# Kernel tuning notes

Measured on AMD Instinct MI355X. Metric: run time of the kernel, lower is better.

Reference implementation:

```python
import jax, jax.numpy as jnp
import numpy as np

N = 20000      # total nodes (100 graphs x 200 nodes)
B = 100        # batch_size
PER = 200      # nodes per graph (uniform) -> max_num_nodes
E = 320000     # edges (before self-loops)
F_IN = 32      # num_features
HEADS = 10
OUT = 128      # output_dim
NEG_SLOPE = 0.2  # PyG GATConv default


def setup_inputs() -> dict:
    key = jax.random.key(0)
    ks = jax.random.split(key, 14)
    feats = jax.random.normal(ks[0], (N, F_IN), jnp.float32)
    src = jax.random.randint(ks[1], (E,), 0, N)
    dst = jax.random.randint(ks[2], (E,), 0, N)
    edge_index = jnp.stack([src, dst]).astype(jnp.int32)
    graph_id = jnp.repeat(jnp.arange(B, dtype=jnp.int32), PER)
    batch_num_nodes = jnp.full((B,), PER, jnp.int32)
    s1 = 1.0 / np.sqrt(F_IN)
    s2 = 1.0 / np.sqrt(F_IN * HEADS)
    s3 = 1.0 / np.sqrt(OUT)
    return {
        "feats": feats,
        "edge_index": edge_index,
        "graph_id": graph_id,
        "batch_num_nodes": batch_num_nodes,
        # GATConv 1: in F_IN -> HEADS x F_IN, concat
        "W1": jax.random.normal(ks[3], (F_IN, HEADS * F_IN), jnp.float32) * s1,
        "a1_src": jax.random.normal(ks[4], (HEADS, F_IN), jnp.float32) * s1,
        "a1_dst": jax.random.normal(ks[5], (HEADS, F_IN), jnp.float32) * s1,
        "b1": jnp.zeros((HEADS * F_IN,), jnp.float32),
        "W2": jax.random.normal(ks[6], (HEADS * F_IN, OUT), jnp.float32) * s2,
        "a2_src": jax.random.normal(ks[7], (1, OUT), jnp.float32) * s3,
        "a2_dst": jax.random.normal(ks[8], (1, OUT), jnp.float32) * s3,
        "b2": jnp.zeros((OUT,), jnp.float32),
        # shared fc_g1
        "fc_w": jax.random.normal(ks[9], (OUT, OUT), jnp.float32) * s3,
        "fc_b": jnp.zeros((OUT,), jnp.float32),
    }


def gat_conv(x, src, dst, W, a_src, a_dst, bias, heads, out_dim):
    # x: [N, Fin]; src/dst already include self-loops (PyG default add_self_loops=True)
    n = x.shape[0]
    xw = (x @ W).reshape(n, heads, out_dim)                 # [N,H,F]
    s_src = jnp.einsum('nhf,hf->nh', xw, a_src)             # [N,H]
    s_dst = jnp.einsum('nhf,hf->nh', xw, a_dst)
    e = jax.nn.leaky_relu(s_src[src] + s_dst[dst], NEG_SLOPE)  # [E,H]
    # segment softmax over incoming edges of each destination node
    m = jax.ops.segment_max(e, dst, num_segments=n)         # [N,H]
    ex = jnp.exp(e - m[dst])
    denom = jax.ops.segment_sum(ex, dst, num_segments=n)    # [N,H]
    alpha = ex / jnp.maximum(denom[dst], 1e-16)             # [E,H]
    out = jax.ops.segment_sum(alpha[:, :, None] * xw[src], dst, num_segments=n)  # [N,H,F]
    return out.reshape(n, heads * out_dim) + bias


def reference(feats, edge_index, graph_id, batch_num_nodes,
              W1, a1_src, a1_dst, b1, W2, a2_src, a2_dst, b2, fc_w, fc_b):
    n = feats.shape[0]
    loops = jnp.arange(n, dtype=edge_index.dtype)
    src = jnp.concatenate([edge_index[0], loops])
    dst = jnp.concatenate([edge_index[1], loops])
    x = feats.astype(jnp.float32)
    # dropout layers are identity in eval mode
    x = jax.nn.elu(gat_conv(x, src, dst, W1, a1_src, a1_dst, b1, HEADS, F_IN))
    x = gat_conv(x, src, dst, W2, a2_src, a2_dst, b2, 1, OUT)
    x = jax.nn.relu(x)                                       # [N, OUT]
    # dgl_split: scatter node feats into [B, max_num_nodes, OUT] padded tensor
    cum = jnp.concatenate([jnp.zeros((1,), jnp.int32),
                           jnp.cumsum(batch_num_nodes).astype(jnp.int32)])
    idx = jnp.arange(n, dtype=jnp.int32) - cum[graph_id] + graph_id * PER
    padded = jnp.zeros((B * PER, OUT), x.dtype).at[idx].set(x).reshape(B, PER, OUT)
    out = jax.nn.relu(padded @ fc_w + fc_b)                  # [B, PER, OUT]
    # global max pool per graph, then shared fc_g1 + relu
    pooled = jax.ops.segment_max(x, graph_id, num_segments=B)  # [B, OUT]
    pooled = jax.nn.relu(pooled @ fc_w + fc_b)
    return (out, pooled)
```

## Files before the change

kernel.cpp:

```cpp
#include <hip/hip_runtime.h>

#define N_NODES 20000
#define N_EDGES 320000
#define ETOT    (N_EDGES + N_NODES)
#define HEADS   10
#define F_IN    32
#define C1      (HEADS * F_IN)
#define C2      128
#define NB      100
#define PER     200
#define CAP     96
#define SSTRIDE 12
#define HSTRIDE 328
#define X2STRIDE 136

typedef __attribute__((ext_vector_type(8))) short bf16x8;
typedef __attribute__((ext_vector_type(4))) float floatx4;
typedef _Float16 f16;
typedef _Float16 f16x2 __attribute__((ext_vector_type(2)));
typedef _Float16 f16x4 __attribute__((ext_vector_type(4)));
typedef _Float16 f16x8 __attribute__((ext_vector_type(8)));

static __device__ __forceinline__ unsigned short f2bf(float f) {
    unsigned int u = __float_as_uint(f);
    unsigned int r = (u + 0x7fffu + ((u >> 16) & 1u)) >> 16;
    return (unsigned short)r;
}

#define SCAT_BLOCKS  ((ETOT + 255) / 256)
#define SCORE_BLOCKS ((N_NODES + 63) / 64)
#define W2P_BLOCKS   ((C1 * C2 + 255) / 256)
#define W1P_BLOCKS   ((HEADS * F_IN * F_IN + 255) / 256)
#define FCP_BLOCKS   ((C2 * C2 + 255) / 256)
#define F16_BLOCKS   ((N_NODES * F_IN / 4 + 255) / 256)
__global__ __launch_bounds__(256) void mega_prep_kernel(
        const int* __restrict__ ei, int* __restrict__ cursor, int* __restrict__ csr_src,
        const float* __restrict__ feats, f16* __restrict__ feats16,
        const float* __restrict__ W1, unsigned short* __restrict__ W1p,
        const float* __restrict__ W2, unsigned short* __restrict__ W2p,
        const float* __restrict__ fcw, f16* __restrict__ FCp,
        const float* __restrict__ a1s, const float* __restrict__ a1d,
        float* __restrict__ s_src, float* __restrict__ s_dst) {
    unsigned int b = blockIdx.x;
    if (b < SCAT_BLOCKS) {
        int e = b * 256 + threadIdx.x;
        if (e >= ETOT) return;
        int s, d;
        if (e < N_EDGES) { s = ei[e]; d = ei[N_EDGES + e]; }
        else             { s = e - N_EDGES; d = s; }
        int pos = atomicAdd(&cursor[d], 1);
        csr_src[(size_t)d * CAP + pos] = s;
        return;
    }
    b -= SCAT_BLOCKS;
    if (b < SCORE_BLOCKS) {
        __shared__ __align__(16) float A[64 * F_IN];
        __shared__ float Ws[C1], Wd[C1];
        int t = threadIdx.x;
        for (int o = t; o < C1; o += 256) {
            int k = o & 31, h = o >> 5;
            float ss = 0.f, dd = 0.f;
#pragma unroll
            for (int f = 0; f < F_IN; f++) {
                float wv = W1[k * C1 + h * 32 + f];
                ss += wv * a1s[h * 32 + f];
                dd += wv * a1d[h * 32 + f];
            }
            Ws[k * HEADS + h] = ss;
            Wd[k * HEADS + h] = dd;
        }
        int n0 = b * 64;
        int nrows = min(64, N_NODES - n0);
        const float4* fs = (const float4*)(feats + (size_t)n0 * F_IN);
        float4* Af = (float4*)A;
        for (int i = t; i < nrows * 8; i += 256) Af[i] = fs[i];
        __syncthreads();
        for (int o = t; o < nrows * HEADS; o += 256) {
            int nl = o / HEADS, h = o - nl * HEADS;
            const float* ar = A + nl * F_IN;
            float ss = 0.f, dd = 0.f;
#pragma unroll
            for (int k = 0; k < F_IN; k++) {
                float av = ar[k];
                ss += av * Ws[k * HEADS + h];
                dd += av * Wd[k * HEADS + h];
            }
            s_src[(size_t)(n0 + nl) * SSTRIDE + h] = ss;
            s_dst[(size_t)(n0 + nl) * SSTRIDE + h] = dd;
        }
        return;
    }
    b -= SCORE_BLOCKS;
    if (b < W2P_BLOCKS) {
        int o = b * 256 + threadIdx.x;
        if (o >= C1 * C2) return;
        int j    = o & 7;
        int lane = (o >> 3) & 63;
        int ct   = (o >> 9) & 7;
        int kb   = o >> 12;
        int k = kb * 32 + (lane >> 4) * 8 + j;
        int n = ct * 16 + (lane & 15);
        W2p[o] = f2bf(W2[k * C2 + n]);
        return;
    }
    b -= W2P_BLOCKS;
    if (b < W1P_BLOCKS) {
        int o = b * 256 + threadIdx.x;
        if (o >= HEADS * F_IN * F_IN) return;
        int j    = o & 7;
        int lane = (o >> 3) & 63;
        int ct   = (o >> 9) & 1;
        int h    = o >> 10;
        int k = (lane >> 4) * 8 + j;
        int f = ct * 16 + (lane & 15);
        W1p[o] = f2bf(W1[k * C1 + h * 32 + f]);
        return;
    }
    b -= W1P_BLOCKS;
    if (b < FCP_BLOCKS) {
        int o = b * 256 + threadIdx.x;
        if (o >= C2 * C2) return;
        int j    = o & 7;
        int lane = (o >> 3) & 63;
        int ct   = (o >> 9) & 7;
        int kb   = o >> 12;
        int k = kb * 32 + (lane >> 4) * 8 + j;
        int n = ct * 16 + (lane & 15);
        FCp[o] = (f16)fcw[k * C2 + n];
        return;
    }
    b -= FCP_BLOCKS;
    {
        int o = b * 256 + threadIdx.x;
        if (o < N_NODES * F_IN / 4) {
            float4 v = ((const float4*)feats)[o];
            f16* d = feats16 + 4 * o;
            d[0] = (f16)v.x; d[1] = (f16)v.y; d[2] = (f16)v.z; d[3] = (f16)v.w;
        }
    }
}

__global__ __launch_bounds__(512) void agg1h1g2_kernel(
        const f16* __restrict__ feats16, const float* __restrict__ s_src,
        const float* __restrict__ s_dst, const int* __restrict__ deg_arr,
        const int* __restrict__ csr_src,
        const unsigned short* __restrict__ W1p, const float* __restrict__ b1,
        const unsigned short* __restrict__ W2p,
        const float* __restrict__ a_src, const float* __restrict__ a_dst,
        f16* __restrict__ xw2h, float* __restrict__ s_src2, float* __restrict__ s_dst2) {
    union Smem {
        struct { f16 P[16][HEADS * 32]; int S[16][32]; } p1;
        unsigned short H[16 * HSTRIDE];
    };
    __shared__ __align__(16) Smem u;
    __shared__ __align__(16) unsigned short G[16 * HSTRIDE];
    __shared__ float redS[8][16], redD[8][16];

    int tid   = threadIdx.x;
    int wslot = tid >> 6;
    int lane  = tid & 63;
    int r     = tid >> 5;
    int l     = tid & 31;
    int row0  = blockIdx.x * 16;
    f16* P = u.p1.P[r];
    int* S = u.p1.S[r];
    const f16x2 ones = {(f16)1.f, (f16)1.f};
    const char* fb = (const char*)feats16 + 2 * l;

    {
        int n = row0 + r;
        int beg = n * CAP, deg = deg_arr[n];
        const float* sdp = s_dst + (size_t)n * SSTRIDE;
        float sd[10];
        {
            float4 v0 = *(const float4*)(sdp);
            float4 v1 = *(const float4*)(sdp + 4);
            float2 v2 = *(const float2*)(sdp + 8);
            sd[0]=v0.x; sd[1]=v0.y; sd[2]=v0.z; sd[3]=v0.w;
            sd[4]=v1.x; sd[5]=v1.y; sd[6]=v1.z; sd[7]=v1.w;
            sd[8]=v2.x; sd[9]=v2.y;
        }
        float g[10], la[10];
#pragma unroll
        for (int h = 0; h < 10; h++) { g[h] = 0.f; la[h] = 0.f; }

        for (int c0 = 0; c0 < deg; c0 += 32) {
            int dc = min(deg - c0, 32);
            bool act = l < dc;
            int s_e = csr_src[beg + c0 + min(l, dc - 1)];
            const float* ssp = s_src + (size_t)s_e * SSTRIDE;
            float ss[10];
            {
                float4 v0 = *(const float4*)(ssp);
                float4 v1 = *(const float4*)(ssp + 4);
                float2 v2 = *(const float2*)(ssp + 8);
                ss[0]=v0.x; ss[1]=v0.y; ss[2]=v0.z; ss[3]=v0.w;
                ss[4]=v1.x; ss[5]=v1.y; ss[6]=v1.z; ss[7]=v1.w;
                ss[8]=v2.x; ss[9]=v2.y;
            }
            float p[10];
#pragma unroll
            for (int h = 0; h < 10; h++) {
                float e0 = ss[h] + sd[h];
                e0 = (e0 >= 0.f) ? e0 : 0.2f * e0;
                p[h] = act ? __expf(e0) : 0.f;
            }
            S[l] = s_e << 6;
#pragma unroll
            for (int h = 0; h < 10; h++) P[h * 32 + l] = (f16)p[h];
            asm volatile("s_waitcnt lgkmcnt(0)" ::: "memory");

            int dcp = (dc + 3) & ~3;
            for (int i = 0; i < dcp; i += 4) {
                int4 ss4 = *(const int4*)&S[i];
                f16x2 v01, v23;
                v01.x = *(const f16*)(fb + ss4.x);
                v01.y = *(const f16*)(fb + ss4.y);
                v23.x = *(const f16*)(fb + ss4.z);
                v23.y = *(const f16*)(fb + ss4.w);
#pragma unroll
                for (int h = 0; h < 10; h++) {
                    f16x4 pp = *(const f16x4*)&P[h * 32 + i];
                    f16x2 p01 = {pp[0], pp[1]};
                    f16x2 p23 = {pp[2], pp[3]};
                    g[h]  = __builtin_amdgcn_fdot2(p01, v01, g[h], false);
                    g[h]  = __builtin_amdgcn_fdot2(p23, v23, g[h], false);
                    la[h] = __builtin_amdgcn_fdot2(p01, ones, la[h], false);
                    la[h] = __builtin_amdgcn_fdot2(p23, ones, la[h], false);
                }
            }
            asm volatile("s_waitcnt lgkmcnt(0)" ::: "memory");
        }
        unsigned short* gr = &G[r * HSTRIDE + l];
#pragma unroll
        for (int h = 0; h < 10; h++)
            gr[h * 32] = f2bf(g[h] / fmaxf(la[h], 1e-16f));
    }
    __syncthreads();

    int quad = lane >> 4, col = lane & 15;
    for (int h = wslot; h < 10; h += 8) {
        bf16x8 a = *(const bf16x8*)&G[col * HSTRIDE + h * 32 + quad * 8];
        bf16x8 bA = ((const bf16x8*)W1p)[(h * 2 + 0) * 64 + lane];
        bf16x8 bB = ((const bf16x8*)W1p)[(h * 2 + 1) * 64 + lane];
        floatx4 z = {0.f, 0.f, 0.f, 0.f};
        floatx4 c0 = __builtin_amdgcn_mfma_f32_16x16x32_bf16(a, bA, z, 0, 0, 0);
        floatx4 c1 = __builtin_amdgcn_mfma_f32_16x16x32_bf16(a, bB, z, 0, 0, 0);
        float bias0 = b1[h * 32 + col];
        float bias1 = b1[h * 32 + 16 + col];
#pragma unroll
        for (int reg = 0; reg < 4; reg++) {
            int rr = quad * 4 + reg;
            float o0 = c0[reg] + bias0;
            float o1 = c1[reg] + bias1;
            o0 = (o0 > 0.f) ? o0 : (__expf(o0) - 1.f);
            o1 = (o1 > 0.f) ? o1 : (__expf(o1) - 1.f);
            u.H[rr * HSTRIDE + h * 32 + col]      = f2bf(o0);
            u.H[rr * HSTRIDE + h * 32 + 16 + col] = f2bf(o1);
        }
    }
    __syncthreads();

    floatx4 acc = {0.f, 0.f, 0.f, 0.f};
    const bf16x8* pb = (const bf16x8*)W2p;
#pragma unroll
    for (int kb = 0; kb < 10; kb++) {
        bf16x8 a = *(const bf16x8*)&u.H[col * HSTRIDE + kb * 32 + quad * 8];
        bf16x8 b = pb[(kb * 8 + wslot) * 64 + lane];
        acc = __builtin_amdgcn_mfma_f32_16x16x32_bf16(a, b, acc, 0, 0, 0);
    }
    float asv = a_src[wslot * 16 + col];
    float adv = a_dst[wslot * 16 + col];
#pragma unroll
    for (int reg = 0; reg < 4; reg++) {
        int row = row0 + quad * 4 + reg;
        float v = acc[reg];
        xw2h[(size_t)row * C2 + wslot * 16 + col] = (f16)v;
        float vs = v * asv, vd = v * adv;
#pragma unroll
        for (int off = 8; off >= 1; off >>= 1) {
            vs += __shfl_xor(vs, off);
            vd += __shfl_xor(vd, off);
        }
        if (col == 0) { redS[wslot][quad * 4 + reg] = vs; redD[wslot][quad * 4 + reg] = vd; }
    }
    __syncthreads();
    if (wslot == 0) {
        if (lane < 16) {
            float s = 0.f;
#pragma unroll
            for (int w2 = 0; w2 < 8; w2++) s += redS[w2][lane];
            s_src2[row0 + lane] = s;
        } else if (lane < 32) {
            int r2 = lane - 16;
            float d = 0.f;
#pragma unroll
            for (int w2 = 0; w2 < 8; w2++) d += redD[w2][r2];
            s_dst2[row0 + r2] = d;
        }
    }
}

template <int PASS>
__global__ __launch_bounds__(512) void agg2pass_kernel(
        const f16* __restrict__ xw2h, const float* __restrict__ s_src2,
        const float* __restrict__ s_dst2, const int* __restrict__ deg_arr,
        const int* __restrict__ csr_src, const float* __restrict__ b2,
        f16* __restrict__ Xh0, const f16* __restrict__ FCp,
        const float* __restrict__ fcb,
        float* __restrict__ out, int* __restrict__ pooledi) {
    __shared__ __align__(16) int2 shE[16][32];
    __shared__ __align__(16) f16 X[16 * X2STRIDE];
    int tid   = threadIdx.x;
    int wslot = tid >> 6;
    int lane  = tid & 63;
    int r     = tid >> 5;
    int l     = tid & 31;
    int row0  = blockIdx.x * 16;
    int2* E = shE[r];
    const char* xb = (const char*)xw2h + PASS * 128 + 4 * l;

    {
        int n = row0 + r;
        int beg = n * CAP, deg = deg_arr[n];
        float sd = s_dst2[n];
        float ldn = 0.f, a0 = 0.f, a1 = 0.f;

        for (int c0 = 0; c0 < deg; c0 += 32) {
            int dc = min(deg - c0, 32);
            bool act = l < dc;
            int s_e = csr_src[beg + c0 + min(l, dc - 1)];
            float e = s_src2[s_e] + sd;
            e = (e >= 0.f) ? e : 0.2f * e;
            float p = act ? __expf(e) : 0.f;
            float su = p;
#pragma unroll
            for (int off = 16; off >= 1; off >>= 1) su += __shfl_xor(su, off);
            ldn += su;

            E[l] = make_int2(s_e << 8, __float_as_int(p));
            asm volatile("s_waitcnt lgkmcnt(0)" ::: "memory");

            int dcr = (dc + 3) & ~3;
            for (int i = 0; i < dcr; i += 4) {
                int4 e01 = *(const int4*)&E[i];
                int4 e23 = *(const int4*)&E[i + 2];
                f16x2 v0 = *(const f16x2*)(xb + e01.x);
                f16x2 v1 = *(const f16x2*)(xb + e01.z);
                f16x2 v2 = *(const f16x2*)(xb + e23.x);
                f16x2 v3 = *(const f16x2*)(xb + e23.z);
                float p0 = __int_as_float(e01.y), p1 = __int_as_float(e01.w);
                float p2 = __int_as_float(e23.y), p3 = __int_as_float(e23.w);
                a0 += p0 * (float)v0.x + p1 * (float)v1.x + p2 * (float)v2.x + p3 * (float)v3.x;
                a1 += p0 * (float)v0.y + p1 * (float)v1.y + p2 * (float)v2.y + p3 * (float)v3.y;
            }
            asm volatile("s_waitcnt lgkmcnt(0)" ::: "memory");
        }

        float linv = 1.f / fmaxf(ldn, 1e-16f);
        float2 bb = *(const float2*)(b2 + PASS * 64 + 2 * l);
        f16x2 o;
        o.x = (f16)fmaxf(a0 * linv + bb.x, 0.f);
        o.y = (f16)fmaxf(a1 * linv + bb.y, 0.f);
        if (PASS == 0) {
            *(f16x2*)&Xh0[(size_t)n * 64 + 2 * l] = o;
        } else {
            *(f16x2*)&X[r * X2STRIDE + 64 + 2 * l] = o;
            *(f16x2*)&X[r * X2STRIDE + 2 * l] =
                *(const f16x2*)&Xh0[(size_t)(row0 + r) * 64 + 2 * l];
        }
    }
    if (PASS == 0) return;
    __syncthreads();

    int quad = lane >> 4, col = lane & 15;
    floatx4 acc = {0.f, 0.f, 0.f, 0.f};
    const f16x8* pb = (const f16x8*)FCp;
#pragma unroll
    for (int kb = 0; kb < 4; kb++) {
        f16x8 a = *(const f16x8*)&X[col * X2STRIDE + kb * 32 + quad * 8];
        f16x8 b = pb[(kb * 8 + wslot) * 64 + lane];
        acc = __builtin_amdgcn_mfma_f32_16x16x32_f16(a, b, acc, 0, 0, 0);
    }
    float bias = fcb[wslot * 16 + col];
#pragma unroll
    for (int reg = 0; reg < 4; reg++) {
        int row = row0 + quad * 4 + reg;
        out[(size_t)row * C2 + wslot * 16 + col] = fmaxf(acc[reg] + bias, 0.f);
    }

    if (tid < C2) {
        int c = tid;
        int gA = row0 / PER;
        int gB = (row0 + 15) / PER;
        float mA = 0.f, mB = 0.f;
#pragma unroll
        for (int rr = 0; rr < 16; rr++) {
            float v = (float)X[rr * X2STRIDE + c];
            if ((row0 + rr) / PER == gA) mA = fmaxf(mA, v);
            else                         mB = fmaxf(mB, v);
        }
        atomicMax(&pooledi[gA * C2 + c], __float_as_int(mA));
        if (gB != gA) atomicMax(&pooledi[gB * C2 + c], __float_as_int(mB));
    }
}

__global__ void poolfc_kernel(const int* __restrict__ pooledi, const float* __restrict__ fcw,
                              const float* __restrict__ fcb, float* __restrict__ outp) {
    __shared__ float mx[C2];
    int g = blockIdx.x, t = threadIdx.x;
    mx[t] = __int_as_float(pooledi[g * C2 + t]);
    __syncthreads();
    float acc = 0.f;
    for (int k = 0; k < C2; k++) acc += mx[k] * fcw[k * C2 + t];
    outp[g * C2 + t] = fmaxf(acc + fcb[t], 0.f);
}

extern "C" void kernel_launch(void* const* d_in, const int* in_sizes, int n_in,
                              void* d_out, int out_size, void* d_ws, size_t ws_size,
                              hipStream_t stream) {
    const float* feats = (const float*)d_in[0];
    const int*   ei    = (const int*)d_in[1];
    const float* W1  = (const float*)d_in[4];
    const float* a1s = (const float*)d_in[5];
    const float* a1d = (const float*)d_in[6];
    const float* b1  = (const float*)d_in[7];
    const float* W2  = (const float*)d_in[8];
    const float* a2s = (const float*)d_in[9];
    const float* a2d = (const float*)d_in[10];
    const float* b2  = (const float*)d_in[11];
    const float* fcw = (const float*)d_in[12];
    const float* fcb = (const float*)d_in[13];

    float* out_main = (float*)d_out;
    float* out_pool = (float*)d_out + (size_t)N_NODES * C2;

    char* p = (char*)d_ws;
    auto alloc = [&](size_t bytes) {
        char* r = p;
        p += (bytes + 255) & ~(size_t)255;
        return r;
    };
    unsigned short* W2p  = (unsigned short*)alloc(sizeof(short) * C1 * C2);
    unsigned short* W1p  = (unsigned short*)alloc(sizeof(short) * HEADS * F_IN * F_IN);
    f16*   FCp     = (f16*)alloc(sizeof(f16) * C2 * C2);
    f16*   feats16 = (f16*)alloc(sizeof(f16) * (size_t)N_NODES * F_IN);
    f16*   xw2h    = (f16*)alloc(sizeof(f16) * (size_t)N_NODES * C2);
    f16*   Xh0     = (f16*)alloc(sizeof(f16) * (size_t)N_NODES * 64);
    float* s1s    = (float*)alloc(sizeof(float) * N_NODES * SSTRIDE);
    float* s1d    = (float*)alloc(sizeof(float) * N_NODES * SSTRIDE);
    float* s2s    = (float*)alloc(sizeof(float) * N_NODES);
    float* s2d    = (float*)alloc(sizeof(float) * N_NODES);
    const int NZ = N_NODES + NB * C2;
    int* zeros   = (int*)alloc(sizeof(int) * NZ);
    int* cursor  = zeros;
    int* pooledi = zeros + N_NODES;
    int* csr_src = (int*)alloc(sizeof(int) * N_NODES * CAP);

    hipMemsetAsync(zeros, 0, sizeof(int) * NZ, stream);

    mega_prep_kernel<<<SCAT_BLOCKS + SCORE_BLOCKS + W2P_BLOCKS + W1P_BLOCKS + FCP_BLOCKS + F16_BLOCKS,
                       256, 0, stream>>>(
        ei, cursor, csr_src, feats, feats16, W1, W1p, W2, W2p, fcw, FCp,
        a1s, a1d, s1s, s1d);

    agg1h1g2_kernel<<<1250, 512, 0, stream>>>(feats16, s1s, s1d, cursor, csr_src,
                                              W1p, b1, W2p, a2s, a2d, xw2h, s2s, s2d);
    agg2pass_kernel<0><<<1250, 512, 0, stream>>>(xw2h, s2s, s2d, cursor, csr_src, b2,
                                                 Xh0, FCp, fcb, out_main, pooledi);
    agg2pass_kernel<1><<<1250, 512, 0, stream>>>(xw2h, s2s, s2d, cursor, csr_src, b2,
                                                 Xh0, FCp, fcb, out_main, pooledi);
    poolfc_kernel<<<NB, C2, 0, stream>>>(pooledi, fcw, fcb, out_pool);
}
```

Measured before the change: 158.7 us.

## Fuse two-pass layer-2 aggregation into one kernel and fully unroll gather loops

Merges the two half-column aggregation passes into a single kernel in which each lane gathers four f16 columns with a wider load. This drops the Xh0 intermediate buffer and one kernel launch, and the edge list and softmax weights are computed only once. The inner gather loops in both aggregation kernels are also fully unrolled to 32 entries. Entries beyond the degree then carry zero weight but still issue loads, which adds wasted gathers for low-degree nodes.

```diff
diff --git a/kernel.cpp b/kernel.cpp
--- a/kernel.cpp
+++ b/kernel.cpp
@@ -210,8 +210,8 @@
             for (int h = 0; h < 10; h++) P[h * 32 + l] = (f16)p[h];
             asm volatile("s_waitcnt lgkmcnt(0)" ::: "memory");
 
-            int dcp = (dc + 3) & ~3;
-            for (int i = 0; i < dcp; i += 4) {
+#pragma unroll
+            for (int i = 0; i < 32; i += 4) {
                 int4 ss4 = *(const int4*)&S[i];
                 f16x2 v01, v23;
                 v01.x = *(const f16*)(fb + ss4.x);
@@ -301,13 +301,11 @@
     }
 }
 
-template <int PASS>
-__global__ __launch_bounds__(512) void agg2pass_kernel(
+__global__ __launch_bounds__(512) void agg2fc_kernel(
         const f16* __restrict__ xw2h, const float* __restrict__ s_src2,
         const float* __restrict__ s_dst2, const int* __restrict__ deg_arr,
         const int* __restrict__ csr_src, const float* __restrict__ b2,
-        f16* __restrict__ Xh0, const f16* __restrict__ FCp,
-        const float* __restrict__ fcb,
+        const f16* __restrict__ FCp, const float* __restrict__ fcb,
         float* __restrict__ out, int* __restrict__ pooledi) {
     __shared__ __align__(16) int2 shE[16][32];
     __shared__ __align__(16) f16 X[16 * X2STRIDE];
@@ -318,13 +316,13 @@
     int l     = tid & 31;
     int row0  = blockIdx.x * 16;
     int2* E = shE[r];
-    const char* xb = (const char*)xw2h + PASS * 128 + 4 * l;
+    const char* xb = (const char*)xw2h + 8 * l;
 
     {
         int n = row0 + r;
         int beg = n * CAP, deg = deg_arr[n];
         float sd = s_dst2[n];
-        float ldn = 0.f, a0 = 0.f, a1 = 0.f;
+        float ldn = 0.f, a0 = 0.f, a1 = 0.f, a2 = 0.f, a3 = 0.f;
 
         for (int c0 = 0; c0 < deg; c0 += 32) {
             int dc = min(deg - c0, 32);
@@ -341,36 +339,33 @@
             E[l] = make_int2(s_e << 8, __float_as_int(p));
             asm volatile("s_waitcnt lgkmcnt(0)" ::: "memory");
 
-            int dcr = (dc + 3) & ~3;
-            for (int i = 0; i < dcr; i += 4) {
+#pragma unroll
+            for (int i = 0; i < 32; i += 4) {
                 int4 e01 = *(const int4*)&E[i];
                 int4 e23 = *(const int4*)&E[i + 2];
-                f16x2 v0 = *(const f16x2*)(xb + e01.x);
-                f16x2 v1 = *(const f16x2*)(xb + e01.z);
-                f16x2 v2 = *(const f16x2*)(xb + e23.x);
-                f16x2 v3 = *(const f16x2*)(xb + e23.z);
+                f16x4 v0 = *(const f16x4*)(xb + e01.x);
+                f16x4 v1 = *(const f16x4*)(xb + e01.z);
+                f16x4 v2 = *(const f16x4*)(xb + e23.x);
+                f16x4 v3 = *(const f16x4*)(xb + e23.z);
                 float p0 = __int_as_float(e01.y), p1 = __int_as_float(e01.w);
                 float p2 = __int_as_float(e23.y), p3 = __int_as_float(e23.w);
-                a0 += p0 * (float)v0.x + p1 * (float)v1.x + p2 * (float)v2.x + p3 * (float)v3.x;
-                a1 += p0 * (float)v0.y + p1 * (float)v1.y + p2 * (float)v2.y + p3 * (float)v3.y;
+                a0 += p0 * (float)v0[0] + p1 * (float)v1[0] + p2 * (float)v2[0] + p3 * (float)v3[0];
+                a1 += p0 * (float)v0[1] + p1 * (float)v1[1] + p2 * (float)v2[1] + p3 * (float)v3[1];
+                a2 += p0 * (float)v0[2] + p1 * (float)v1[2] + p2 * (float)v2[2] + p3 * (float)v3[2];
+                a3 += p0 * (float)v0[3] + p1 * (float)v1[3] + p2 * (float)v2[3] + p3 * (float)v3[3];
             }
             asm volatile("s_waitcnt lgkmcnt(0)" ::: "memory");
         }
 
         float linv = 1.f / fmaxf(ldn, 1e-16f);
-        float2 bb = *(const float2*)(b2 + PASS * 64 + 2 * l);
-        f16x2 o;
-        o.x = (f16)fmaxf(a0 * linv + bb.x, 0.f);
-        o.y = (f16)fmaxf(a1 * linv + bb.y, 0.f);
-        if (PASS == 0) {
-            *(f16x2*)&Xh0[(size_t)n * 64 + 2 * l] = o;
-        } else {
-            *(f16x2*)&X[r * X2STRIDE + 64 + 2 * l] = o;
-            *(f16x2*)&X[r * X2STRIDE + 2 * l] =
-                *(const f16x2*)&Xh0[(size_t)(row0 + r) * 64 + 2 * l];
-        }
-    }
-    if (PASS == 0) return;
+        float4 bb = *(const float4*)(b2 + 4 * l);
+        f16x4 o;
+        o[0] = (f16)fmaxf(a0 * linv + bb.x, 0.f);
+        o[1] = (f16)fmaxf(a1 * linv + bb.y, 0.f);
+        o[2] = (f16)fmaxf(a2 * linv + bb.z, 0.f);
+        o[3] = (f16)fmaxf(a3 * linv + bb.w, 0.f);
+        *(f16x4*)&X[r * X2STRIDE + 4 * l] = o;
+    }
     __syncthreads();
 
     int quad = lane >> 4, col = lane & 15;
@@ -446,7 +441,6 @@
     f16*   FCp     = (f16*)alloc(sizeof(f16) * C2 * C2);
     f16*   feats16 = (f16*)alloc(sizeof(f16) * (size_t)N_NODES * F_IN);
     f16*   xw2h    = (f16*)alloc(sizeof(f16) * (size_t)N_NODES * C2);
-    f16*   Xh0     = (f16*)alloc(sizeof(f16) * (size_t)N_NODES * 64);
     float* s1s    = (float*)alloc(sizeof(float) * N_NODES * SSTRIDE);
     float* s1d    = (float*)alloc(sizeof(float) * N_NODES * SSTRIDE);
     float* s2s    = (float*)alloc(sizeof(float) * N_NODES);
@@ -466,9 +460,7 @@
 
     agg1h1g2_kernel<<<1250, 512, 0, stream>>>(feats16, s1s, s1d, cursor, csr_src,
                                               W1p, b1, W2p, a2s, a2d, xw2h, s2s, s2d);
-    agg2pass_kernel<0><<<1250, 512, 0, stream>>>(xw2h, s2s, s2d, cursor, csr_src, b2,
-                                                 Xh0, FCp, fcb, out_main, pooledi);
-    agg2pass_kernel<1><<<1250, 512, 0, stream>>>(xw2h, s2s, s2d, cursor, csr_src, b2,
-                                                 Xh0, FCp, fcb, out_main, pooledi);
+    agg2fc_kernel<<<1250, 512, 0, stream>>>(xw2h, s2s, s2d, cursor, csr_src, b2,
+                                            FCp, fcb, out_main, pooledi);
     poolfc_kernel<<<NB, C2, 0, stream>>>(pooledi, fcw, fcb, out_pool);
 }
```

Result: no change. 158.9 us (+0.1%).
